# Optimization experiments

Hardware: AMD Instinct MI355X
Metric: run time of the kernel (lower is better)

The kernel has to match this reference:

```python
import jax, jax.numpy as jnp
import numpy as np

N_VISIBLE = 50000
N_HIDDEN = 5000
N_NODES = N_VISIBLE + N_HIDDEN
N_EDGES = 1_000_000
BATCH = 128


def setup_inputs() -> dict:
    key = jax.random.key(0)
    k1, k2, k3, k4, k5 = jax.random.split(key, 5)
    # parameters, initialized as in the torch module
    linear = 0.05 * (2.0 * jax.random.uniform(k1, (N_NODES,), dtype=jnp.float32) - 1.0)
    quadratic = 5.0 * (2.0 * jax.random.uniform(k2, (N_EDGES,), dtype=jnp.float32) - 1.0)
    # bipartite visible-hidden edges -> CSR-like flat buffers (via segment ids)
    flat_adj = jax.random.randint(k3, (N_EDGES,), 0, N_VISIBLE, dtype=jnp.int32).astype(jnp.int64)  # visible endpoint per edge
    seg_ids = jax.random.randint(k4, (N_EDGES,), 0, N_HIDDEN, dtype=jnp.int32).astype(jnp.int64)    # hidden bin per edge
    flat_j_idx = jnp.arange(N_EDGES, dtype=jnp.int64)  # quadratic coefficient index per flat entry
    hidden_idx = jnp.arange(N_HIDDEN, dtype=jnp.int64) + N_VISIBLE
    # observed spin configurations in {0,1} (mapped to +-1 inside reference)
    s = jax.random.randint(k5, (BATCH, N_NODES), 0, 2, dtype=jnp.int32)
    return {
        "linear": linear,
        "quadratic": quadratic,
        "s": s,
        "flat_adj": flat_adj,
        "flat_j_idx": flat_j_idx,
        "seg_ids": seg_ids,
        "hidden_idx": hidden_idx,
        "n_hidden": N_HIDDEN,
    }


def reference(linear, quadratic, s, flat_adj, flat_j_idx, seg_ids, hidden_idx, n_hidden):
    """Per-hidden-unit effective field + conditional spin expectation.

    eff[b, k] = linear[hidden_idx[k]]
                + sum_{e : seg_ids[e]==k} quadratic[flat_j_idx[e]] * s_pm[b, flat_adj[e]]
    returns tanh(-eff)  (conditional expectation of hidden spins given visibles)
    """
    s_pm = (2 * s - 1).astype(linear.dtype)                 # {0,1} -> {-1,+1}, (B, N)
    w = quadratic[flat_j_idx]                               # (E,)
    contrib = s_pm[:, flat_adj].T * w[:, None]              # (E, B) gathered neighbor terms
    field = jax.ops.segment_sum(contrib, seg_ids, num_segments=n_hidden)  # (K, B)
    eff = field.T + linear[hidden_idx][None, :]             # (B, K)
    return jnp.tanh(-eff)
```

## Files before the change

### kernel.cpp

```cpp
#include <hip/hip_runtime.h>
#include <math.h>
#include <stdint.h>

#define NV 50000
#define NH 5000
#define NN 55000
#define NB 128
#define NG 8
#define SUBSLOT 64
#define MAXREC 512


__global__ void pack_s_kernel(const int* __restrict__ s, uint32_t* __restrict__ bits) {
    int tid = blockIdx.x * 256 + threadIdx.x;
    int v = tid >> 2;
    int g = tid & 3;
    if (v >= NV) return;
    const int* col = s + (size_t)g * 32 * NN + v;
    uint32_t w = 0;
#pragma unroll
    for (int j = 0; j < 32; ++j)
        w |= (uint32_t)(col[(size_t)j * NN] & 1) << j;
    bits[(size_t)v * 4 + g] = w;
}

__global__ void scatter_edges_kernel(const int4* __restrict__ adj4,
                                     const int4* __restrict__ seg4,
                                     const float4* __restrict__ quad4,
                                     uint32_t* __restrict__ cursors,
                                     uint2* __restrict__ recs, int E4) {
    int t = blockIdx.x * 256 + threadIdx.x;
    if (t >= E4) return;
    const int g = blockIdx.x & (NG - 1);
    uint32_t* gcur = cursors + (size_t)g * NH;
    uint2* grecs = recs + (size_t)g * NH * SUBSLOT;
    int4 a  = adj4[t];
    int4 sg = seg4[t];
    float4 w = quad4[t];
    uint32_t p0 = atomicAdd(&gcur[sg.x], 1u);
    uint32_t p1 = atomicAdd(&gcur[sg.y], 1u);
    uint32_t p2 = atomicAdd(&gcur[sg.z], 1u);
    uint32_t p3 = atomicAdd(&gcur[sg.w], 1u);
    if (p0 < SUBSLOT) grecs[(size_t)sg.x * SUBSLOT + p0] = make_uint2((uint32_t)a.x, __float_as_uint(w.x));
    if (p1 < SUBSLOT) grecs[(size_t)sg.y * SUBSLOT + p1] = make_uint2((uint32_t)a.y, __float_as_uint(w.y));
    if (p2 < SUBSLOT) grecs[(size_t)sg.z * SUBSLOT + p2] = make_uint2((uint32_t)a.z, __float_as_uint(w.z));
    if (p3 < SUBSLOT) grecs[(size_t)sg.w * SUBSLOT + p3] = make_uint2((uint32_t)a.w, __float_as_uint(w.w));
}

__global__ void __launch_bounds__(256) field_tanh_kernel(
        const uint32_t* __restrict__ cursors,
        const uint2* __restrict__ recs,
        const uint4* __restrict__ bits4,
        const float* __restrict__ linear,
        float* __restrict__ out) {
    int k = (blockIdx.x >> 3) + 625 * (blockIdx.x & 7);
    int tid = threadIdx.x;

    __shared__ __align__(16) uint32_t rows[5][MAXREC];
    __shared__ float part[256];

    int c[NG], offs[NG];
    int T = 0;
#pragma unroll
    for (int g = 0; g < NG; ++g) {
        int cg = (int)cursors[(size_t)g * NH + k];
        if (cg > SUBSLOT) cg = SUBSLOT;
        c[g] = cg;
        offs[g] = T;
        T += cg;
    }
    int T8 = (T + 7) & ~7;

    if (tid < T8 - T) rows[4][T + tid] = 0u;

    int lane = tid & 63;
#pragma unroll
    for (int p = 0; p < 2; ++p) {
        int g = (tid >> 6) * 2 + p;
        if (lane < c[g]) {
            uint2 r = recs[((size_t)g * NH + k) * SUBSLOT + lane];
            uint4 m = bits4[r.x];
            int idx = offs[g] + lane;
            rows[0][idx] = m.x;
            rows[1][idx] = m.y;
            rows[2][idx] = m.z;
            rows[3][idx] = m.w;
            rows[4][idx] = r.y;
        }
    }
    __syncthreads();

    int b = tid & 127;
    int grp = tid >> 7;
    const uint32_t* mrow = rows[(b >> 5) & 3];
    const uint32_t* wrow = rows[4];
    const int bsh = b & 31;
    float a0 = 0.f, a1 = 0.f, a2 = 0.f, a3 = 0.f;
    for (int i = grp * 4; i < T8; i += 8) {
        uint4 mm = *(const uint4*)(mrow + i);
        uint4 ww = *(const uint4*)(wrow + i);
        float f0 = __uint_as_float(ww.x);
        float f1 = __uint_as_float(ww.y);
        float f2 = __uint_as_float(ww.z);
        float f3 = __uint_as_float(ww.w);
        a0 += ((mm.x >> bsh) & 1u) ? f0 : -f0;
        a1 += ((mm.y >> bsh) & 1u) ? f1 : -f1;
        a2 += ((mm.z >> bsh) & 1u) ? f2 : -f2;
        a3 += ((mm.w >> bsh) & 1u) ? f3 : -f3;
    }
    part[tid] = (a0 + a1) + (a2 + a3);
    __syncthreads();
    if (tid < 128) {
        float eff = part[tid] + part[tid + 128] + linear[NV + k];
        out[(size_t)tid * NH + k] = tanhf(-eff);
    }
}

extern "C" void kernel_launch(void* const* d_in, const int* in_sizes, int n_in,
                              void* d_out, int out_size, void* d_ws, size_t ws_size,
                              hipStream_t stream) {
    const float* linear = (const float*)d_in[0];
    const float* quad   = (const float*)d_in[1];
    const int*   s      = (const int*)d_in[2];
    const int*   adj    = (const int*)d_in[3];
    const int*   seg    = (const int*)d_in[5];
    const int E = in_sizes[5];
    float* out = (float*)d_out;

    char* ws = (char*)d_ws;
    uint32_t* bits    = (uint32_t*)(ws);
    uint32_t* cursors = (uint32_t*)(ws + 800000);
    uint2*    recs    = (uint2*)   (ws + 960000);

    hipMemsetAsync(cursors, 0, NH * NG * sizeof(uint32_t), stream);
    pack_s_kernel<<<(NV * 4 + 255) / 256, 256, 0, stream>>>(s, bits);
    const int E4 = E / 4;
    scatter_edges_kernel<<<(E4 + 255) / 256, 256, 0, stream>>>(
        (const int4*)adj, (const int4*)seg, (const float4*)quad, cursors, recs, E4);
    field_tanh_kernel<<<NH, 256, 0, stream>>>(cursors, recs, (const uint4*)bits, linear, out);
}
```

Measured before the change: 157.6 us.

## Fuse pack and scatter kernels; process two hidden units per block

Merges the bit-packing and edge-scatter kernels into one launch, with block ranges split by index, so the two independent phases can overlap and one launch is saved. The field kernel now handles two adjacent hidden units per block, doubling shared memory and writing float2 outputs. The record gather now loops over a flat index and walks the group counts to find each entry. This halves the number of field blocks but raises shared memory per block, which may lower occupancy.

```diff
diff --git a/kernel.cpp b/kernel.cpp
--- a/kernel.cpp
+++ b/kernel.cpp
@@ -11,40 +11,42 @@
 #define MAXREC 512
 
 
-__global__ void pack_s_kernel(const int* __restrict__ s, uint32_t* __restrict__ bits) {
-    int tid = blockIdx.x * 256 + threadIdx.x;
-    int v = tid >> 2;
-    int g = tid & 3;
-    if (v >= NV) return;
-    const int* col = s + (size_t)g * 32 * NN + v;
-    uint32_t w = 0;
+__global__ void __launch_bounds__(256) pack_scatter_kernel(
+        const int* __restrict__ s, uint32_t* __restrict__ bits,
+        const int4* __restrict__ adj4, const int4* __restrict__ seg4,
+        const float4* __restrict__ quad4,
+        uint32_t* __restrict__ cursors, uint2* __restrict__ recs,
+        int packBlocks, int E4) {
+    int blk = blockIdx.x;
+    if (blk < packBlocks) {
+        int tid = blk * 256 + threadIdx.x;
+        int v = tid >> 2;
+        int g = tid & 3;
+        if (v >= NV) return;
+        const int* col = s + (size_t)g * 32 * NN + v;
+        uint32_t w = 0;
 #pragma unroll
-    for (int j = 0; j < 32; ++j)
-        w |= (uint32_t)(col[(size_t)j * NN] & 1) << j;
-    bits[(size_t)v * 4 + g] = w;
-}
-
-__global__ void scatter_edges_kernel(const int4* __restrict__ adj4,
-                                     const int4* __restrict__ seg4,
-                                     const float4* __restrict__ quad4,
-                                     uint32_t* __restrict__ cursors,
-                                     uint2* __restrict__ recs, int E4) {
-    int t = blockIdx.x * 256 + threadIdx.x;
-    if (t >= E4) return;
-    const int g = blockIdx.x & (NG - 1);
-    uint32_t* gcur = cursors + (size_t)g * NH;
-    uint2* grecs = recs + (size_t)g * NH * SUBSLOT;
-    int4 a  = adj4[t];
-    int4 sg = seg4[t];
-    float4 w = quad4[t];
-    uint32_t p0 = atomicAdd(&gcur[sg.x], 1u);
-    uint32_t p1 = atomicAdd(&gcur[sg.y], 1u);
-    uint32_t p2 = atomicAdd(&gcur[sg.z], 1u);
-    uint32_t p3 = atomicAdd(&gcur[sg.w], 1u);
-    if (p0 < SUBSLOT) grecs[(size_t)sg.x * SUBSLOT + p0] = make_uint2((uint32_t)a.x, __float_as_uint(w.x));
-    if (p1 < SUBSLOT) grecs[(size_t)sg.y * SUBSLOT + p1] = make_uint2((uint32_t)a.y, __float_as_uint(w.y));
-    if (p2 < SUBSLOT) grecs[(size_t)sg.z * SUBSLOT + p2] = make_uint2((uint32_t)a.z, __float_as_uint(w.z));
-    if (p3 < SUBSLOT) grecs[(size_t)sg.w * SUBSLOT + p3] = make_uint2((uint32_t)a.w, __float_as_uint(w.w));
+        for (int j = 0; j < 32; ++j)
+            w |= (uint32_t)(col[(size_t)j * NN] & 1) << j;
+        bits[(size_t)v * 4 + g] = w;
+    } else {
+        int t = (blk - packBlocks) * 256 + threadIdx.x;
+        if (t >= E4) return;
+        const int g = blk & (NG - 1);
+        uint32_t* gcur = cursors + (size_t)g * NH;
+        uint2* grecs = recs + (size_t)g * NH * SUBSLOT;
+        int4 a  = adj4[t];
+        int4 sg = seg4[t];
+        float4 w = quad4[t];
+        uint32_t p0 = atomicAdd(&gcur[sg.x], 1u);
+        uint32_t p1 = atomicAdd(&gcur[sg.y], 1u);
+        uint32_t p2 = atomicAdd(&gcur[sg.z], 1u);
+        uint32_t p3 = atomicAdd(&gcur[sg.w], 1u);
+        if (p0 < SUBSLOT) grecs[(size_t)sg.x * SUBSLOT + p0] = make_uint2((uint32_t)a.x, __float_as_uint(w.x));
+        if (p1 < SUBSLOT) grecs[(size_t)sg.y * SUBSLOT + p1] = make_uint2((uint32_t)a.y, __float_as_uint(w.y));
+        if (p2 < SUBSLOT) grecs[(size_t)sg.z * SUBSLOT + p2] = make_uint2((uint32_t)a.z, __float_as_uint(w.z));
+        if (p3 < SUBSLOT) grecs[(size_t)sg.w * SUBSLOT + p3] = make_uint2((uint32_t)a.w, __float_as_uint(w.w));
+    }
 }
 
 __global__ void __launch_bounds__(256) field_tanh_kernel(
@@ -53,66 +55,75 @@
         const uint4* __restrict__ bits4,
         const float* __restrict__ linear,
         float* __restrict__ out) {
-    int k = (blockIdx.x >> 3) + 625 * (blockIdx.x & 7);
+    int g8 = blockIdx.x & 7;
+    int m = blockIdx.x >> 3;
+    int pair = m + 313 * g8;
+    if (pair >= NH / 2) return;
+    int k0 = pair * 2;
     int tid = threadIdx.x;
 
-    __shared__ __align__(16) uint32_t rows[5][MAXREC];
-    __shared__ float part[256];
+    __shared__ __align__(16) uint32_t rows[2][5][MAXREC];
+    __shared__ float part[2][256];
 
-    int c[NG], offs[NG];
-    int T = 0;
+    int T8s[2];
 #pragma unroll
-    for (int g = 0; g < NG; ++g) {
-        int cg = (int)cursors[(size_t)g * NH + k];
-        if (cg > SUBSLOT) cg = SUBSLOT;
-        c[g] = cg;
-        offs[g] = T;
-        T += cg;
-    }
-    int T8 = (T + 7) & ~7;
-
-    if (tid < T8 - T) rows[4][T + tid] = 0u;
-
-    int lane = tid & 63;
+    for (int kk = 0; kk < 2; ++kk) {
+        int k = k0 + kk;
+        int c[NG], offs[NG], T = 0;
 #pragma unroll
-    for (int p = 0; p < 2; ++p) {
-        int g = (tid >> 6) * 2 + p;
-        if (lane < c[g]) {
-            uint2 r = recs[((size_t)g * NH + k) * SUBSLOT + lane];
-            uint4 m = bits4[r.x];
-            int idx = offs[g] + lane;
-            rows[0][idx] = m.x;
-            rows[1][idx] = m.y;
-            rows[2][idx] = m.z;
-            rows[3][idx] = m.w;
-            rows[4][idx] = r.y;
+        for (int g = 0; g < NG; ++g) {
+            int cg = (int)cursors[(size_t)g * NH + k];
+            if (cg > SUBSLOT) cg = SUBSLOT;
+            c[g] = cg;
+            offs[g] = T;
+            T += cg;
+        }
+        int T8 = (T + 7) & ~7;
+        T8s[kk] = T8;
+        for (int i = T + tid; i < T8; i += 256) rows[kk][4][i] = 0u;
+        for (int t = tid; t < T; t += 256) {
+            int rem = t, g = 0;
+            while (rem >= c[g]) { rem -= c[g]; ++g; }
+            uint2 r = recs[((size_t)g * NH + k) * SUBSLOT + rem];
+            uint4 mw = bits4[r.x];
+            rows[kk][0][t] = mw.x;
+            rows[kk][1][t] = mw.y;
+            rows[kk][2][t] = mw.z;
+            rows[kk][3][t] = mw.w;
+            rows[kk][4][t] = r.y;
         }
     }
     __syncthreads();
 
     int b = tid & 127;
     int grp = tid >> 7;
-    const uint32_t* mrow = rows[(b >> 5) & 3];
-    const uint32_t* wrow = rows[4];
     const int bsh = b & 31;
-    float a0 = 0.f, a1 = 0.f, a2 = 0.f, a3 = 0.f;
-    for (int i = grp * 4; i < T8; i += 8) {
-        uint4 mm = *(const uint4*)(mrow + i);
-        uint4 ww = *(const uint4*)(wrow + i);
-        float f0 = __uint_as_float(ww.x);
-        float f1 = __uint_as_float(ww.y);
-        float f2 = __uint_as_float(ww.z);
-        float f3 = __uint_as_float(ww.w);
-        a0 += ((mm.x >> bsh) & 1u) ? f0 : -f0;
-        a1 += ((mm.y >> bsh) & 1u) ? f1 : -f1;
-        a2 += ((mm.z >> bsh) & 1u) ? f2 : -f2;
-        a3 += ((mm.w >> bsh) & 1u) ? f3 : -f3;
+    const int widx = b >> 5;
+#pragma unroll
+    for (int kk = 0; kk < 2; ++kk) {
+        const uint32_t* mrow = rows[kk][widx];
+        const uint32_t* wrow = rows[kk][4];
+        float a0 = 0.f, a1 = 0.f, a2 = 0.f, a3 = 0.f;
+        for (int i = grp * 4; i < T8s[kk]; i += 8) {
+            uint4 mm = *(const uint4*)(mrow + i);
+            uint4 ww = *(const uint4*)(wrow + i);
+            float f0 = __uint_as_float(ww.x);
+            float f1 = __uint_as_float(ww.y);
+            float f2 = __uint_as_float(ww.z);
+            float f3 = __uint_as_float(ww.w);
+            a0 += ((mm.x >> bsh) & 1u) ? f0 : -f0;
+            a1 += ((mm.y >> bsh) & 1u) ? f1 : -f1;
+            a2 += ((mm.z >> bsh) & 1u) ? f2 : -f2;
+            a3 += ((mm.w >> bsh) & 1u) ? f3 : -f3;
+        }
+        part[kk][tid] = (a0 + a1) + (a2 + a3);
     }
-    part[tid] = (a0 + a1) + (a2 + a3);
     __syncthreads();
     if (tid < 128) {
-        float eff = part[tid] + part[tid + 128] + linear[NV + k];
-        out[(size_t)tid * NH + k] = tanhf(-eff);
+        float e0 = part[0][tid] + part[0][tid + 128] + linear[NV + k0];
+        float e1 = part[1][tid] + part[1][tid + 128] + linear[NV + k0 + 1];
+        float2 o = make_float2(tanhf(-e0), tanhf(-e1));
+        *(float2*)(out + (size_t)tid * NH + k0) = o;
     }
 }
 
@@ -133,9 +144,12 @@
     uint2*    recs    = (uint2*)   (ws + 960000);
 
     hipMemsetAsync(cursors, 0, NH * NG * sizeof(uint32_t), stream);
-    pack_s_kernel<<<(NV * 4 + 255) / 256, 256, 0, stream>>>(s, bits);
     const int E4 = E / 4;
-    scatter_edges_kernel<<<(E4 + 255) / 256, 256, 0, stream>>>(
-        (const int4*)adj, (const int4*)seg, (const float4*)quad, cursors, recs, E4);
-    field_tanh_kernel<<<NH, 256, 0, stream>>>(cursors, recs, (const uint4*)bits, linear, out);
+    const int packBlocks = (NV * 4 + 255) / 256;
+    const int scatBlocks = (E4 + 255) / 256;
+    pack_scatter_kernel<<<packBlocks + scatBlocks, 256, 0, stream>>>(
+        s, bits, (const int4*)adj, (const int4*)seg, (const float4*)quad,
+        cursors, recs, packBlocks, E4);
+    field_tanh_kernel<<<313 * 8, 256, 0, stream>>>(cursors, recs, (const uint4*)bits,
+                                                   linear, out);
 }
```

Result: no change. 155.3 us (-1.5%).
